# Kernel optimization log

Measured on AMD Instinct MI355X. Metric: run time of the kernel, lower is better.

## Reference

```python
import jax, jax.numpy as jnp
import numpy as np

FP8_MAX = 448.0  # finfo(float8_e4m3fn).max
EPS = 1e-12
BLK = 128        # weight_block_size = (128, 128); activation group_size = 128


def setup_inputs() -> dict:
    key = jax.random.key(0)
    k1, k2, k3, k4 = jax.random.split(key, 4)
    B, S, H, O = 4, 4096, 2048, 2048
    x = jax.random.normal(k1, (B, S, H), dtype=jnp.float32)
    # fp8 weight: generate, round to e4m3fn grid, store as f32 (values exactly fp8-representable)
    w_raw = jax.random.normal(k2, (O, H), dtype=jnp.float32) * 0.02
    weight = w_raw.astype(jnp.float8_e4m3fn).astype(jnp.float32)
    # per-(128x128)-block weight scales
    weight_scale = jax.random.uniform(k3, (O // BLK, H // BLK), dtype=jnp.float32,
                                      minval=0.001, maxval=0.01)
    bias = jax.random.normal(k4, (O,), dtype=jnp.float32) * 0.01
    return {"x": x, "weight": weight, "weight_scale": weight_scale, "bias": bias}


def reference(x, weight, weight_scale, bias):
    B, S, H = x.shape
    O = weight.shape[0]
    J = H // BLK  # number of activation groups / weight column-blocks
    # per-token-group fp8 quantization (group_size = BLK)
    xg = x.reshape(-1, J, BLK)                                      # [M, J, BLK]
    max_abs = jnp.clip(jnp.max(jnp.abs(xg), axis=-1, keepdims=True), EPS)
    scales = FP8_MAX / max_abs                                      # [M, J, 1]
    xq = jnp.clip(xg * scales, -FP8_MAX, FP8_MAX)
    xq = xq.astype(jnp.float8_e4m3fn).astype(jnp.float32)           # fp8 round-trip
    inv_scale = 1.0 / scales                                        # stored input_scale
    # block-scaled matmul == dequantize both operands then single GEMM
    x_dq = (xq * inv_scale).reshape(-1, H)                          # [M, H]
    w_scale_full = jnp.repeat(jnp.repeat(weight_scale, BLK, axis=0), BLK, axis=1)  # [O, H]
    w_dq = weight * w_scale_full                                    # [O, H]
    y = x_dq @ w_dq.T + bias                                        # [M, O]
    return y.reshape(B, S, O)
```

## Files before the change

### kernel.cpp

```cpp
#include <hip/hip_runtime.h>
#include <cstdint>

#define FP8MAX 448.0f

typedef float f32x4 __attribute__((ext_vector_type(4)));
typedef int   i32x4 __attribute__((ext_vector_type(4)));

__device__ __forceinline__ void gload_lds16(const void* g, void* l) {
  __builtin_amdgcn_global_load_lds(
      (const __attribute__((address_space(1))) unsigned int*)g,
      (__attribute__((address_space(3))) unsigned int*)l,
      16, 0, 0);
}

__global__ __launch_bounds__(256) void quant_x(const float* __restrict__ x,
                                               uint8_t* __restrict__ xq,
                                               float* __restrict__ sa) {
  const int m = blockIdx.x;
  const int t = threadIdx.x;
  const float* xr = x + (size_t)m * 2048;
  float4 v0 = ((const float4*)xr)[t * 2];
  float4 v1 = ((const float4*)xr)[t * 2 + 1];
  float amax = fmaxf(fmaxf(fmaxf(fabsf(v0.x), fabsf(v0.y)), fmaxf(fabsf(v0.z), fabsf(v0.w))),
                     fmaxf(fmaxf(fabsf(v1.x), fabsf(v1.y)), fmaxf(fabsf(v1.z), fabsf(v1.w))));
  #pragma unroll
  for (int off = 1; off < 16; off <<= 1)
    amax = fmaxf(amax, __shfl_xor(amax, off));
  amax = fmaxf(amax, 1e-12f);
  float s   = FP8MAX / amax;
  float inv = 1.0f / s;
  if ((t & 15) == 0) sa[(size_t)m * 16 + (t >> 4)] = inv;
  float q[8] = {v0.x * s, v0.y * s, v0.z * s, v0.w * s,
                v1.x * s, v1.y * s, v1.z * s, v1.w * s};
  #pragma unroll
  for (int i = 0; i < 8; ++i) q[i] = fminf(fmaxf(q[i], -FP8MAX), FP8MAX);
  union { unsigned long long u; unsigned int w[2]; } pk;
  pk.w[0] = __builtin_amdgcn_cvt_pk_fp8_f32(q[0], q[1], 0, false);
  pk.w[0] = __builtin_amdgcn_cvt_pk_fp8_f32(q[2], q[3], pk.w[0], true);
  pk.w[1] = __builtin_amdgcn_cvt_pk_fp8_f32(q[4], q[5], 0, false);
  pk.w[1] = __builtin_amdgcn_cvt_pk_fp8_f32(q[6], q[7], pk.w[1], true);
  ((unsigned long long*)(xq + (size_t)m * 2048))[t] = pk.u;
}

__global__ __launch_bounds__(256) void conv_w(const float* __restrict__ w,
                                              uint8_t* __restrict__ w8, int n8) {
  int i = blockIdx.x * 256 + threadIdx.x;
  if (i >= n8) return;
  float4 v0 = ((const float4*)w)[i * 2];
  float4 v1 = ((const float4*)w)[i * 2 + 1];
  union { unsigned long long u; unsigned int x[2]; } pk;
  pk.x[0] = __builtin_amdgcn_cvt_pk_fp8_f32(v0.x, v0.y, 0, false);
  pk.x[0] = __builtin_amdgcn_cvt_pk_fp8_f32(v0.z, v0.w, pk.x[0], true);
  pk.x[1] = __builtin_amdgcn_cvt_pk_fp8_f32(v1.x, v1.y, 0, false);
  pk.x[1] = __builtin_amdgcn_cvt_pk_fp8_f32(v1.z, v1.w, pk.x[1], true);
  ((unsigned long long*)w8)[i] = pk.u;
}

__global__ __launch_bounds__(256, 2) void gemm_fp8(
    const uint8_t* __restrict__ A, const uint8_t* __restrict__ Bw,
    const float* __restrict__ sa, const float* __restrict__ sb,
    const float* __restrict__ bias, float* __restrict__ out,
    int M, int N, int K) {
  const int J = K >> 7;
  const int nbn = N >> 7;
  const int bn = blockIdx.x % nbn;
  const int bm = blockIdx.x / nbn;
  const int t = threadIdx.x;
  const int lane = t & 63;
  const int w = t >> 6;
  const int wm = (w >> 1) << 6;
  const int wn = (w & 1) << 6;
  const int r16 = lane & 15;
  const int kg = lane >> 4;

  __shared__ __align__(16) uint8_t lA[2][128 * 128];
  __shared__ __align__(16) uint8_t lB[2][128 * 128];
  __shared__ __align__(16) float sal[16 * 128];

  const uint8_t* gA = A + (size_t)bm * 128 * K;
  const uint8_t* gB = Bw + (size_t)bn * 128 * K;

  for (int i = t; i < 128 * 16; i += 256) {
    int row = i >> 4, j = i & 15;
    sal[j * 128 + row] = sa[((size_t)bm * 128 + row) * 16 + j];
  }

  const int srow = t >> 3;
  const int sseg = t & 7;

  #pragma unroll
  for (int it = 0; it < 4; ++it) {
    int r = srow + it * 32;
    int ss = ((sseg ^ (r & 7)) << 4);
    gload_lds16(gA + (size_t)r * K + ss, &lA[0][r * 128 + sseg * 16]);
    gload_lds16(gB + (size_t)r * K + ss, &lB[0][r * 128 + sseg * 16]);
  }
  __syncthreads();

  f32x4 tot[4][4] = {};
  const f32x4 fz = {0.f, 0.f, 0.f, 0.f};

  int rowA[4], rowB[4];
  #pragma unroll
  for (int a = 0; a < 4; ++a) rowA[a] = wm + a * 16 + r16;
  #pragma unroll
  for (int b = 0; b < 4; ++b) rowB[b] = wn + b * 16 + r16;

  int cur = 0;
  const int KT = K >> 7;
  for (int kt = 0; kt < KT; ++kt) {
    if (kt + 1 < KT) {
      const uint8_t* gA2 = gA + (size_t)(kt + 1) * 128;
      const uint8_t* gB2 = gB + (size_t)(kt + 1) * 128;
      #pragma unroll
      for (int it = 0; it < 4; ++it) {
        int r = srow + it * 32;
        int ss = ((sseg ^ (r & 7)) << 4);
        gload_lds16(gA2 + (size_t)r * K + ss, &lA[cur ^ 1][r * 128 + sseg * 16]);
        gload_lds16(gB2 + (size_t)r * K + ss, &lB[cur ^ 1][r * 128 + sseg * 16]);
      }
    }
    f32x4 part[4][4];
    #pragma unroll
    for (int p = 0; p < 2; ++p) {
      i32x4 av[4], bv[4];
      #pragma unroll
      for (int a = 0; a < 4; ++a) {
        int off = (p * 64 + kg * 16) ^ ((rowA[a] & 7) << 4);
        av[a] = *(const i32x4*)&lA[cur][rowA[a] * 128 + off];
      }
      #pragma unroll
      for (int b = 0; b < 4; ++b) {
        int off = (p * 64 + kg * 16) ^ ((rowB[b] & 7) << 4);
        bv[b] = *(const i32x4*)&lB[cur][rowB[b] * 128 + off];
      }
      #pragma unroll
      for (int h = 0; h < 2; ++h) {
        #pragma unroll
        for (int a = 0; a < 4; ++a) {
          union { i32x4 v; long long l[2]; } ua; ua.v = av[a];
          long long aa = ua.l[h];
          #pragma unroll
          for (int b = 0; b < 4; ++b) {
            union { i32x4 v; long long l[2]; } ub; ub.v = bv[b];
            part[a][b] = __builtin_amdgcn_mfma_f32_16x16x32_fp8_fp8(
                aa, ub.l[h], (p == 0 && h == 0) ? fz : part[a][b], 0, 0, 0);
          }
        }
      }
    }
    float sbj = sb[bn * J + kt];
    #pragma unroll
    for (int a = 0; a < 4; ++a) {
      f32x4 sv = *(const f32x4*)&sal[kt * 128 + wm + a * 16 + kg * 4];
      f32x4 sc = sv * sbj;
      #pragma unroll
      for (int b = 0; b < 4; ++b)
        tot[a][b] += part[a][b] * sc;
    }
    __syncthreads();
    cur ^= 1;
  }

  float bb4[4];
  #pragma unroll
  for (int b = 0; b < 4; ++b) bb4[b] = bias[bn * 128 + wn + b * 16 + r16];
  #pragma unroll
  for (int a = 0; a < 4; ++a) {
    int row0 = bm * 128 + wm + a * 16 + kg * 4;
    #pragma unroll
    for (int r = 0; r < 4; ++r) {
      float* orow = out + (size_t)(row0 + r) * N + bn * 128;
      #pragma unroll
      for (int b = 0; b < 4; ++b)
        orow[wn + b * 16 + r16] = tot[a][b][r] + bb4[b];
    }
  }
}

extern "C" void kernel_launch(void* const* d_in, const int* in_sizes, int n_in,
                              void* d_out, int out_size, void* d_ws, size_t ws_size,
                              hipStream_t stream) {
  const float* x    = (const float*)d_in[0];
  const float* wt   = (const float*)d_in[1];
  const float* wsc  = (const float*)d_in[2];
  const float* bias = (const float*)d_in[3];
  float* out = (float*)d_out;

  const int O = in_sizes[3];
  const int H = in_sizes[1] / O;
  const int M = in_sizes[0] / H;

  uint8_t* xq = (uint8_t*)d_ws;
  uint8_t* w8 = xq + (size_t)M * H;
  float*   sa = (float*)(w8 + (size_t)O * H);

  quant_x<<<M, 256, 0, stream>>>(x, xq, sa);
  int n8 = O * H / 8;
  conv_w<<<(n8 + 255) / 256, 256, 0, stream>>>(wt, w8, n8);
  int grid = (M / 128) * (O / 128);
  gemm_fp8<<<grid, 256, 0, stream>>>(xq, w8, sa, wsc, bias, out, M, O, H);
}
```

Baseline: 152.9 us.

## Use 16x16x128 scaled-MFMA for fp8 GEMM, remap blocks across XCDs, pad scale LDS

Each 128-wide K tile now takes one gfx950 mfma_scale_f32_16x16x128_f8f6f4 instruction per output fragment, with unit scales, in place of four 16x16x32 fp8 MFMAs. Each lane loads a contiguous 32-byte fragment from the swizzled LDS tile. Workgroup ids are permuted so consecutive tiles land on the same XCD, which should improve L2 reuse. The activation-scale LDS row is padded from 128 to 132 floats to reduce bank conflicts. The new instruction places K elements across lanes differently, so correctness depends on A and B fragments sharing the same K permutation.

After: 134.1 us. 1.14x faster.

```diff
diff --git a/kernel.cpp b/kernel.cpp
--- a/kernel.cpp
+++ b/kernel.cpp
@@ -5,6 +5,9 @@
 
 typedef float f32x4 __attribute__((ext_vector_type(4)));
 typedef int   i32x4 __attribute__((ext_vector_type(4)));
+typedef int   i32x8 __attribute__((ext_vector_type(8)));
+
+union frag8 { i32x8 v8; i32x4 v4[2]; };
 
 __device__ __forceinline__ void gload_lds16(const void* g, void* l) {
   __builtin_amdgcn_global_load_lds(
@@ -63,8 +66,14 @@
     int M, int N, int K) {
   const int J = K >> 7;
   const int nbn = N >> 7;
-  const int bn = blockIdx.x % nbn;
-  const int bm = blockIdx.x / nbn;
+  int bid = blockIdx.x;
+  int nwg = gridDim.x;
+  if ((nwg & 7) == 0) {
+    int cpx = nwg >> 3;
+    bid = (bid & 7) * cpx + (bid >> 3);
+  }
+  const int bn = bid % nbn;
+  const int bm = bid / nbn;
   const int t = threadIdx.x;
   const int lane = t & 63;
   const int w = t >> 6;
@@ -75,14 +84,14 @@
 
   __shared__ __align__(16) uint8_t lA[2][128 * 128];
   __shared__ __align__(16) uint8_t lB[2][128 * 128];
-  __shared__ __align__(16) float sal[16 * 128];
+  __shared__ __align__(16) float sal[16 * 132];
 
   const uint8_t* gA = A + (size_t)bm * 128 * K;
   const uint8_t* gB = Bw + (size_t)bn * 128 * K;
 
   for (int i = t; i < 128 * 16; i += 256) {
     int row = i >> 4, j = i & 15;
-    sal[j * 128 + row] = sa[((size_t)bm * 128 + row) * 16 + j];
+    sal[j * 132 + row] = sa[((size_t)bm * 128 + row) * 16 + j];
   }
 
   const int srow = t >> 3;
@@ -120,43 +129,32 @@
         gload_lds16(gB2 + (size_t)r * K + ss, &lB[cur ^ 1][r * 128 + sseg * 16]);
       }
     }
-    f32x4 part[4][4];
-    #pragma unroll
-    for (int p = 0; p < 2; ++p) {
-      i32x4 av[4], bv[4];
-      #pragma unroll
-      for (int a = 0; a < 4; ++a) {
-        int off = (p * 64 + kg * 16) ^ ((rowA[a] & 7) << 4);
-        av[a] = *(const i32x4*)&lA[cur][rowA[a] * 128 + off];
-      }
+    frag8 av[4], bv[4];
+    #pragma unroll
+    for (int a = 0; a < 4; ++a) {
+      const int swz = (rowA[a] & 7) << 4;
+      const uint8_t* base = &lA[cur][rowA[a] * 128];
+      av[a].v4[0] = *(const i32x4*)(base + ((kg * 32) ^ swz));
+      av[a].v4[1] = *(const i32x4*)(base + ((kg * 32 + 16) ^ swz));
+    }
+    #pragma unroll
+    for (int b = 0; b < 4; ++b) {
+      const int swz = (rowB[b] & 7) << 4;
+      const uint8_t* base = &lB[cur][rowB[b] * 128];
+      bv[b].v4[0] = *(const i32x4*)(base + ((kg * 32) ^ swz));
+      bv[b].v4[1] = *(const i32x4*)(base + ((kg * 32 + 16) ^ swz));
+    }
+    const float sbj = sb[bn * J + kt];
+    #pragma unroll
+    for (int a = 0; a < 4; ++a) {
+      f32x4 sc = *(const f32x4*)&sal[kt * 132 + wm + a * 16 + kg * 4];
+      sc *= sbj;
       #pragma unroll
       for (int b = 0; b < 4; ++b) {
-        int off = (p * 64 + kg * 16) ^ ((rowB[b] & 7) << 4);
-        bv[b] = *(const i32x4*)&lB[cur][rowB[b] * 128 + off];
+        f32x4 part = __builtin_amdgcn_mfma_scale_f32_16x16x128_f8f6f4(
+            av[a].v8, bv[b].v8, fz, 0, 0, 0, 0x7f7f7f7f, 0, 0x7f7f7f7f);
+        tot[a][b] += part * sc;
       }
-      #pragma unroll
-      for (int h = 0; h < 2; ++h) {
-        #pragma unroll
-        for (int a = 0; a < 4; ++a) {
-          union { i32x4 v; long long l[2]; } ua; ua.v = av[a];
-          long long aa = ua.l[h];
-          #pragma unroll
-          for (int b = 0; b < 4; ++b) {
-            union { i32x4 v; long long l[2]; } ub; ub.v = bv[b];
-            part[a][b] = __builtin_amdgcn_mfma_f32_16x16x32_fp8_fp8(
-                aa, ub.l[h], (p == 0 && h == 0) ? fz : part[a][b], 0, 0, 0);
-          }
-        }
-      }
-    }
-    float sbj = sb[bn * J + kt];
-    #pragma unroll
-    for (int a = 0; a < 4; ++a) {
-      f32x4 sv = *(const f32x4*)&sal[kt * 128 + wm + a * 16 + kg * 4];
-      f32x4 sc = sv * sbj;
-      #pragma unroll
-      for (int b = 0; b < 4; ++b)
-        tot[a][b] += part[a][b] * sc;
     }
     __syncthreads();
     cur ^= 1;
```
